# Performance work log

Measured on AMD Instinct MI355X. Metric: run time of the kernel, lower is better.

## Reference

```python
import jax, jax.numpy as jnp
import numpy as np


def setup_inputs() -> dict:
    key = jax.random.key(0)
    k1, k2 = jax.random.split(key)
    B, C, H, W_ = 16, 512, 64, 64
    x = jax.random.normal(k1, (B, C, H, W_), dtype=jnp.float32)
    W = jax.random.normal(k2, (C, C), dtype=jnp.float32) * (1.0 / np.sqrt(C))
    return {"x": x, "W": W}


def reference(x, W):
    B, C, H, Wd = x.shape
    hw = H * Wd
    x1 = x.reshape(B, C, hw)                      # [B, C, HW]
    # linearW applied to x1^T: [B, HW, C] @ W^T -> [B, HW, C]
    x1_corr = jnp.einsum('bch,dc->bhd', x1, W)    # [B, HW, C]
    s = jnp.einsum('bch,bhd->bcd', x1, x1_corr)   # [B, C, C]
    a = jax.nn.softmax(s, axis=2)
    a = jax.nn.softmax(a, axis=1)
    out = jnp.einsum('bcd,bdh->bch', a, x1) + x1  # [B, C, HW]
    return out.reshape(B, C, H, Wd)
```

## Files before the change

kernel.cpp:

```cpp
#include <hip/hip_runtime.h>


typedef __attribute__((ext_vector_type(8))) short bf16x8;
typedef __attribute__((ext_vector_type(4))) float f32x4;

#define DEVINL __device__ __forceinline__
#define CFENCE() asm volatile("" ::: "memory")

DEVINL unsigned short f2bf(float f) {
  union { float f; unsigned int u; } c; c.f = f;
  unsigned int u = c.u;
  u += 0x7fffu + ((u >> 16) & 1u);
  return (unsigned short)(u >> 16);
}

DEVINL float bf2f(unsigned short h) {
  union { unsigned int u; float f; } c; c.u = ((unsigned int)h) << 16;
  return c.f;
}

DEVINL void gld_lds16(const unsigned short* g, unsigned short* l) {
  __builtin_amdgcn_global_load_lds(
      (const __attribute__((address_space(1))) unsigned int*)g,
      (__attribute__((address_space(3))) unsigned int*)l,
      16 , 0, 0);
}

template<int N> DEVINL void vm_wait() {
  if constexpr (N == 0)       asm volatile("s_waitcnt vmcnt(0)" ::: "memory");
  else if constexpr (N == 2)  asm volatile("s_waitcnt vmcnt(2)" ::: "memory");
  else if constexpr (N == 4)  asm volatile("s_waitcnt vmcnt(4)" ::: "memory");
  else if constexpr (N == 8)  asm volatile("s_waitcnt vmcnt(8)" ::: "memory");
  else static_assert(N < 0, "unsupported vmcnt");
}

DEVINL void sym_tile_decode(int t, int& tm, int& tn) {
  if (t < 4)      { tm = 0; tn = t; }
  else if (t < 7) { tm = 1; tn = t - 3; }
  else if (t < 9) { tm = 2; tn = t - 5; }
  else            { tm = 3; tn = 3; }
}

__global__ __launch_bounds__(256)
void cvt_kernel(const float* __restrict__ in, unsigned short* __restrict__ out, int n4) {
  int i = blockIdx.x * 256 + threadIdx.x;
  const int stride = gridDim.x * 256;
  for (; i < n4; i += stride) {
    float4 v = ((const float4*)in)[i];
    unsigned int lo = (unsigned int)f2bf(v.x) | ((unsigned int)f2bf(v.y) << 16);
    unsigned int hi = (unsigned int)f2bf(v.z) | ((unsigned int)f2bf(v.w) << 16);
    uint2 o; o.x = lo; o.y = hi;
    ((uint2*)out)[i] = o;
  }
}

__global__ __launch_bounds__(256)
void fused_cvt_transpose(const float* __restrict__ x, unsigned short* __restrict__ x_bf,
                         unsigned short* __restrict__ xT) {
  __shared__ unsigned int T[2][32][68];
  const int tid = threadIdx.x;
  const int b  = blockIdx.y;
  const int hs = blockIdx.x & 31;
  const int ct = blockIdx.x >> 5;
  const int h0 = hs * 128;
  const int hq = tid & 7;
  const int c2 = tid >> 3;

  uint4 pa[2], pb[2];
  long long rowA[2];
  #pragma unroll
  for (int hh = 0; hh < 2; ++hh) {
    const int hcol = h0 + hh * 64 + hq * 8;
    rowA[hh] = (long long)(b * 512 + ct * 64 + 2 * c2) * 4096 + hcol;
    float4 a0 = *(const float4*)(x + rowA[hh]);
    float4 a1 = *(const float4*)(x + rowA[hh] + 4);
    float4 b0 = *(const float4*)(x + rowA[hh] + 4096);
    float4 b1 = *(const float4*)(x + rowA[hh] + 4100);
    unsigned short ha[8], hb[8];
    ha[0]=f2bf(a0.x); ha[1]=f2bf(a0.y); ha[2]=f2bf(a0.z); ha[3]=f2bf(a0.w);
    ha[4]=f2bf(a1.x); ha[5]=f2bf(a1.y); ha[6]=f2bf(a1.z); ha[7]=f2bf(a1.w);
    hb[0]=f2bf(b0.x); hb[1]=f2bf(b0.y); hb[2]=f2bf(b0.z); hb[3]=f2bf(b0.w);
    hb[4]=f2bf(b1.x); hb[5]=f2bf(b1.y); hb[6]=f2bf(b1.z); hb[7]=f2bf(b1.w);
    pa[hh].x = (unsigned int)ha[0] | ((unsigned int)ha[1] << 16);
    pa[hh].y = (unsigned int)ha[2] | ((unsigned int)ha[3] << 16);
    pa[hh].z = (unsigned int)ha[4] | ((unsigned int)ha[5] << 16);
    pa[hh].w = (unsigned int)ha[6] | ((unsigned int)ha[7] << 16);
    pb[hh].x = (unsigned int)hb[0] | ((unsigned int)hb[1] << 16);
    pb[hh].y = (unsigned int)hb[2] | ((unsigned int)hb[3] << 16);
    pb[hh].z = (unsigned int)hb[4] | ((unsigned int)hb[5] << 16);
    pb[hh].w = (unsigned int)hb[6] | ((unsigned int)hb[7] << 16);
    uint4 u0, u1;
    u0.x = (unsigned int)ha[0] | ((unsigned int)hb[0] << 16);
    u0.y = (unsigned int)ha[1] | ((unsigned int)hb[1] << 16);
    u0.z = (unsigned int)ha[2] | ((unsigned int)hb[2] << 16);
    u0.w = (unsigned int)ha[3] | ((unsigned int)hb[3] << 16);
    u1.x = (unsigned int)ha[4] | ((unsigned int)hb[4] << 16);
    u1.y = (unsigned int)ha[5] | ((unsigned int)hb[5] << 16);
    u1.z = (unsigned int)ha[6] | ((unsigned int)hb[6] << 16);
    u1.w = (unsigned int)ha[7] | ((unsigned int)hb[7] << 16);
    *(uint4*)&T[hh][c2][hq * 8]     = u0;
    *(uint4*)&T[hh][c2][hq * 8 + 4] = u1;
  }
  asm volatile("s_waitcnt lgkmcnt(0)" ::: "memory");
  __builtin_amdgcn_s_barrier();
  #pragma unroll
  for (int hh = 0; hh < 2; ++hh) {
    *(uint4*)(x_bf + rowA[hh])        = pa[hh];
    *(uint4*)(x_bf + rowA[hh] + 4096) = pb[hh];
  }
  const int hh2 = tid >> 7;
  const int h4  = (tid >> 3) & 15;
  const int c8  = tid & 7;
  unsigned int rv[4][4];
  #pragma unroll
  for (int i = 0; i < 4; ++i) {
    uint4 t = *(const uint4*)&T[hh2][c8 * 4 + i][h4 * 4];
    rv[i][0] = t.x; rv[i][1] = t.y; rv[i][2] = t.z; rv[i][3] = t.w;
  }
  #pragma unroll
  for (int r = 0; r < 4; ++r) {
    uint4 o;
    o.x = rv[0][r]; o.y = rv[1][r]; o.z = rv[2][r]; o.w = rv[3][r];
    *(uint4*)(xT + ((long long)(b * 4096 + h0 + hh2 * 64 + h4 * 4 + r) * 512
                    + ct * 64 + c8 * 8)) = o;
  }
}

__global__ __launch_bounds__(256)
void gemm_gsym(const unsigned short* __restrict__ X, unsigned short* __restrict__ P) {
  constexpr int HALF = 128 * 32;
  __shared__ unsigned short As[3 * HALF];
  __shared__ unsigned short Bs[3 * HALF];
  const int tid = threadIdx.x;
  const int l   = tid & 63;
  const int w   = tid >> 6;
  const int wr  = w >> 1, wc = w & 1;
  const int b   = blockIdx.y;
  const int t   = blockIdx.x >> 2;
  const int split = blockIdx.x & 3;
  int tm, tn; sym_tile_decode(t, tm, tn);

  const unsigned short* Ab = X + (long long)b * 2097152 + (long long)(tm * 128) * 4096;
  const unsigned short* Bb = X + (long long)b * 2097152 + (long long)(tn * 128) * 4096;

  f32x4 acc[4][4];
  #pragma unroll
  for (int m = 0; m < 4; ++m)
    #pragma unroll
    for (int n = 0; n < 4; ++n) acc[m][n] = (f32x4){0.f, 0.f, 0.f, 0.f};

  const int srow = tid >> 2;
  const int scol = ((tid & 3) ^ ((tid >> 3) & 3)) * 8;
  const int ch8  = (((l >> 4) ^ ((l >> 1) & 3)) * 8);

  auto stage = [&](int buf, int k0) {
    #pragma unroll
    for (int i = 0; i < 2; ++i)
      gld_lds16(Ab + (long long)(i * 64 + srow) * 4096 + k0 + scol, &As[buf * HALF + i * 2048 + tid * 8]);
    #pragma unroll
    for (int i = 0; i < 2; ++i)
      gld_lds16(Bb + (long long)(i * 64 + srow) * 4096 + k0 + scol, &Bs[buf * HALF + i * 2048 + tid * 8]);
  };
  auto compute = [&](int buf) {
    bf16x8 af[4], bfr[4];
    #pragma unroll
    for (int m = 0; m < 4; ++m)
      af[m] = *(const bf16x8*)&As[buf * HALF + (wr * 64 + m * 16 + (l & 15)) * 32 + ch8];
    #pragma unroll
    for (int n = 0; n < 4; ++n)
      bfr[n] = *(const bf16x8*)&Bs[buf * HALF + (wc * 64 + n * 16 + (l & 15)) * 32 + ch8];
    __builtin_amdgcn_s_setprio(1);
    #pragma unroll
    for (int m = 0; m < 4; ++m)
      #pragma unroll
      for (int n = 0; n < 4; ++n)
        acc[m][n] = __builtin_amdgcn_mfma_f32_16x16x32_bf16(af[m], bfr[n], acc[m][n], 0, 0, 0);
    __builtin_amdgcn_s_setprio(0);
  };

  const int k_beg = split * 1024;
  constexpr int NK = 32;
  stage(0, k_beg);
  stage(1, k_beg + 32);
  int cb = 0, sbuf = 2, ks = k_beg + 64;
  for (int k = 0; k < NK - 2; ++k) {
    stage(sbuf, ks);
    ks += 32;
    sbuf = (sbuf == 2) ? 0 : sbuf + 1;
    vm_wait<8>();
    CFENCE(); __builtin_amdgcn_s_barrier(); CFENCE();
    compute(cb);
    CFENCE(); __builtin_amdgcn_s_barrier(); CFENCE();
    cb = (cb == 2) ? 0 : cb + 1;
  }
  vm_wait<4>();
  CFENCE(); __builtin_amdgcn_s_barrier(); CFENCE();
  compute(cb);
  cb = (cb == 2) ? 0 : cb + 1;
  vm_wait<0>();
  CFENCE(); __builtin_amdgcn_s_barrier(); CFENCE();
  compute(cb);

  unsigned short* Pt = P + (((long long)b * 10 + t) * 4 + split) * 16384;
  const int cc = l & 15, r4 = (l >> 4) * 4;
  #pragma unroll
  for (int m = 0; m < 4; ++m) {
    #pragma unroll
    for (int n = 0; n < 4; ++n) {
      const int row = wr * 64 + m * 16 + r4;
      const int col = wc * 64 + n * 16 + cc;
      #pragma unroll
      for (int j = 0; j < 4; ++j)
        Pt[(row + j) * 128 + col] = f2bf(acc[m][n][j]);
    }
  }
}

__global__ __launch_bounds__(256)
void reduce_mirror(const unsigned short* __restrict__ P, unsigned short* __restrict__ G) {
  __shared__ unsigned short T[128 * 129];
  const int tid = threadIdx.x;
  const int b = blockIdx.y;
  const int t = blockIdx.x;
  int tm, tn; sym_tile_decode(t, tm, tn);
  const unsigned short* Pt = P + ((long long)(b * 10 + t) * 4) * 16384;
  unsigned short* Gb = G + (long long)b * 262144;

  #pragma unroll
  for (int e = 0; e < 16; ++e) {
    const int v = e * 256 + tid;
    ushort4 s0 = ((const ushort4*)Pt)[v];
    ushort4 s1 = ((const ushort4*)(Pt + 16384))[v];
    ushort4 s2 = ((const ushort4*)(Pt + 32768))[v];
    ushort4 s3 = ((const ushort4*)(Pt + 49152))[v];
    unsigned int h0 = f2bf(bf2f(s0.x) + bf2f(s1.x) + bf2f(s2.x) + bf2f(s3.x));
    unsigned int h1 = f2bf(bf2f(s0.y) + bf2f(s1.y) + bf2f(s2.y) + bf2f(s3.y));
    unsigned int h2 = f2bf(bf2f(s0.z) + bf2f(s1.z) + bf2f(s2.z) + bf2f(s3.z));
    unsigned int h3 = f2bf(bf2f(s0.w) + bf2f(s1.w) + bf2f(s2.w) + bf2f(s3.w));
    const int idx = v * 4;
    const int r = idx >> 7, c = idx & 127;
    unsigned int* gp = (unsigned int*)(Gb + (long long)(tm * 128 + r) * 512 + tn * 128 + c);
    gp[0] = h0 | (h1 << 16);
    gp[1] = h2 | (h3 << 16);
    unsigned short* tp = &T[r * 129 + c];
    tp[0] = (unsigned short)h0; tp[1] = (unsigned short)h1;
    tp[2] = (unsigned short)h2; tp[3] = (unsigned short)h3;
  }
  if (tm != tn) {
    __syncthreads();
    #pragma unroll
    for (int e = 0; e < 16; ++e) {
      const int idx = (e * 256 + tid) * 4;
      const int r = idx >> 7, c = idx & 127;
      unsigned int o0 = T[(c + 0) * 129 + r], o1 = T[(c + 1) * 129 + r];
      unsigned int o2 = T[(c + 2) * 129 + r], o3 = T[(c + 3) * 129 + r];
      unsigned int* gp = (unsigned int*)(Gb + (long long)(tn * 128 + r) * 512 + tm * 128 + c);
      gp[0] = o0 | (o1 << 16);
      gp[1] = o2 | (o3 << 16);
    }
  }
}

template<int FR>
__global__ __launch_bounds__(256)
void gemm_bt4(const unsigned short* __restrict__ A, const unsigned short* __restrict__ B,
              float* __restrict__ C,
              int N, int K, int sA, int sB,
              long long bsA, long long bsB, long long bsC, int Ntiles) {
  constexpr int BMN = FR * 32;
  constexpr int ISS = BMN / 64;
  constexpr int HALF = BMN * 32;
  constexpr int NLOAD = 2 * ISS;
  __shared__ unsigned short As[3 * HALF];
  __shared__ unsigned short Bs[3 * HALF];

  const int tid = threadIdx.x;
  const int l   = tid & 63;
  const int w   = tid >> 6;
  const int wr  = w >> 1, wc = w & 1;
  const int bz  = blockIdx.y;
  const int tm  = blockIdx.x / Ntiles;
  const int tn  = blockIdx.x % Ntiles;

  const unsigned short* Ab = A + bz * bsA + (long long)(tm * BMN) * sA;
  const unsigned short* Bb = B + bz * bsB + (long long)(tn * BMN) * sB;

  f32x4 acc[FR][FR];
  #pragma unroll
  for (int m = 0; m < FR; ++m)
    #pragma unroll
    for (int n = 0; n < FR; ++n) acc[m][n] = (f32x4){0.f, 0.f, 0.f, 0.f};

  const int srow = tid >> 2;
  const int scol = ((tid & 3) ^ ((tid >> 3) & 3)) * 8;
  const int ch8  = (((l >> 4) ^ ((l >> 1) & 3)) * 8);

  auto stage = [&](int buf, int k0) {
    #pragma unroll
    for (int i = 0; i < ISS; ++i)
      gld_lds16(Ab + (long long)(i * 64 + srow) * sA + k0 + scol, &As[buf * HALF + i * 2048 + tid * 8]);
    #pragma unroll
    for (int i = 0; i < ISS; ++i)
      gld_lds16(Bb + (long long)(i * 64 + srow) * sB + k0 + scol, &Bs[buf * HALF + i * 2048 + tid * 8]);
  };
  auto compute = [&](int buf) {
    bf16x8 af[FR], bfr[FR];
    #pragma unroll
    for (int m = 0; m < FR; ++m)
      af[m] = *(const bf16x8*)&As[buf * HALF + (wr * (FR * 16) + m * 16 + (l & 15)) * 32 + ch8];
    #pragma unroll
    for (int n = 0; n < FR; ++n)
      bfr[n] = *(const bf16x8*)&Bs[buf * HALF + (wc * (FR * 16) + n * 16 + (l & 15)) * 32 + ch8];
    __builtin_amdgcn_s_setprio(1);
    #pragma unroll
    for (int m = 0; m < FR; ++m)
      #pragma unroll
      for (int n = 0; n < FR; ++n)
        acc[m][n] = __builtin_amdgcn_mfma_f32_16x16x32_bf16(af[m], bfr[n], acc[m][n], 0, 0, 0);
    __builtin_amdgcn_s_setprio(0);
  };

  const int nk = K >> 5;
  stage(0, 0);
  stage(1, 32);
  int cb = 0, sbuf = 2, ks = 64;
  for (int k = 0; k < nk - 2; ++k) {
    stage(sbuf, ks);
    ks += 32;
    sbuf = (sbuf == 2) ? 0 : sbuf + 1;
    vm_wait<2 * NLOAD>();
    CFENCE(); __builtin_amdgcn_s_barrier(); CFENCE();
    compute(cb);
    CFENCE(); __builtin_amdgcn_s_barrier(); CFENCE();
    cb = (cb == 2) ? 0 : cb + 1;
  }
  vm_wait<NLOAD>();
  CFENCE(); __builtin_amdgcn_s_barrier(); CFENCE();
  compute(cb);
  cb = (cb == 2) ? 0 : cb + 1;
  vm_wait<0>();
  CFENCE(); __builtin_amdgcn_s_barrier(); CFENCE();
  compute(cb);

  const int cc = l & 15, r4 = (l >> 4) * 4;
  const int row0 = tm * BMN + wr * (FR * 16);
  const int col0 = tn * BMN + wc * (FR * 16);
  #pragma unroll
  for (int m = 0; m < FR; ++m) {
    #pragma unroll
    for (int n = 0; n < FR; ++n) {
      const int row = row0 + m * 16 + r4;
      const int col = col0 + n * 16 + cc;
      long long base = bz * bsC + (long long)row * N + col;
      #pragma unroll
      for (int j = 0; j < 4; ++j)
        C[base + (long long)j * N] = acc[m][n][j];
    }
  }
}

__global__ __launch_bounds__(256)
void row_softmax_kernel(const float* __restrict__ s, unsigned short* __restrict__ p_bf) {
  __shared__ float red[4], red2[4];
  const float* p = s + (long long)blockIdx.x * 512;
  unsigned short* q = p_bf + (long long)blockIdx.x * 512;
  const int tid = threadIdx.x;
  float v0 = p[tid], v1 = p[tid + 256];
  float m = fmaxf(v0, v1);
  #pragma unroll
  for (int i = 1; i < 64; i <<= 1) m = fmaxf(m, __shfl_xor(m, i));
  if ((tid & 63) == 0) red[tid >> 6] = m;
  __syncthreads();
  m = fmaxf(fmaxf(red[0], red[1]), fmaxf(red[2], red[3]));
  float e0 = __expf(v0 - m), e1 = __expf(v1 - m);
  float sum = e0 + e1;
  #pragma unroll
  for (int i = 1; i < 64; i <<= 1) sum += __shfl_xor(sum, i);
  if ((tid & 63) == 0) red2[tid >> 6] = sum;
  __syncthreads();
  sum = (red2[0] + red2[1]) + (red2[2] + red2[3]);
  float inv = 1.0f / sum;
  q[tid] = f2bf(e0 * inv);
  q[tid + 256] = f2bf(e1 * inv);
}

__global__ __launch_bounds__(256)
void col_softmax_kernel(const unsigned short* __restrict__ p_bf, unsigned short* __restrict__ a_bf) {
  __shared__ float cs[8][32];
  const int tid = threadIdx.x;
  const int dl = tid & 31;
  const int st = tid >> 5;
  const int d  = blockIdx.x * 32 + dl;
  const long long base = (long long)blockIdx.y * 262144 + d;
  const unsigned short* p = p_bf + base;
  float sum = 0.f;
  #pragma unroll 4
  for (int c = st * 64; c < st * 64 + 64; ++c)
    sum += __expf(bf2f(p[(long long)c * 512]));
  cs[st][dl] = sum;
  __syncthreads();
  if (st == 0) {
    float s = ((cs[0][dl] + cs[1][dl]) + (cs[2][dl] + cs[3][dl]))
            + ((cs[4][dl] + cs[5][dl]) + (cs[6][dl] + cs[7][dl]));
    cs[0][dl] = 1.0f / s;
  }
  __syncthreads();
  const float inv = cs[0][dl];
  unsigned short* q = a_bf + base;
  #pragma unroll 4
  for (int c = st * 64; c < st * 64 + 64; ++c) {
    float v = __expf(bf2f(p[(long long)c * 512])) * inv;
    if (c == d) v += 1.0f;
    q[(long long)c * 512] = f2bf(v);
  }
}

extern "C" void kernel_launch(void* const* d_in, const int* in_sizes, int n_in,
                              void* d_out, int out_size, void* d_ws, size_t ws_size,
                              hipStream_t stream) {
  (void)in_sizes; (void)n_in; (void)out_size; (void)ws_size;
  const float* x = (const float*)d_in[0];
  const float* W = (const float*)d_in[1];
  float* out = (float*)d_out;
  char* ws = (char*)d_ws;

  unsigned short* x_bf = (unsigned short*)d_out;
  unsigned short* P = (unsigned short*)((char*)d_out + 67108864);
  unsigned short* p_bf = (unsigned short*)((char*)d_out + 88080384);

  unsigned short* xT   = (unsigned short*)ws;
  unsigned short* G_bf = (unsigned short*)(ws + 67108864);
  float*          s_f  = (float*)(ws + 75497472);
  unsigned short* W_bf = (unsigned short*)(ws + 92274688);
  unsigned short* a_bf = G_bf;

  fused_cvt_transpose<<<dim3(256, 16), 256, 0, stream>>>(x, x_bf, xT);
  cvt_kernel<<<256, 256, 0, stream>>>(W, W_bf, 65536);

  gemm_gsym<<<dim3(40, 16), 256, 0, stream>>>(x_bf, P);

  reduce_mirror<<<dim3(10, 16), 256, 0, stream>>>(P, G_bf);

  gemm_bt4<2><<<dim3(64, 16), 256, 0, stream>>>(
      G_bf, W_bf, s_f,
      512, 512, 512, 512, 262144LL, 0LL, 262144LL, 8);

  row_softmax_kernel<<<8192, 256, 0, stream>>>(s_f, p_bf);
  col_softmax_kernel<<<dim3(16, 16), 256, 0, stream>>>(p_bf, a_bf);

  gemm_bt4<4><<<dim3(128, 16), 256, 0, stream>>>(
      a_bf, xT, out,
      4096, 512, 512, 512, 262144LL, 2097152LL, 2097152LL, 32);
}
```

Before: 183.9 us.

## Switch GEMM pipelines to double-buffered LDS and add nontemporal stores

The two GEMM kernels (gemm_gsym and gemm_bt4) move from a three-buffer shared-memory ring to two buffers. Each iteration now waits for the current tile, computes it, then issues the load for the tile two steps ahead into the buffer it just freed. This cuts LDS use per block, which can let more blocks run on each CU, but leaves less time to hide global-load latency. Separately, the transposed-x writes and the final large fp32 output writes now use nontemporal stores to reduce cache pollution from write-once streams.

```diff
diff --git a/kernel.cpp b/kernel.cpp
--- a/kernel.cpp
+++ b/kernel.cpp
@@ -3,6 +3,7 @@
 
 typedef __attribute__((ext_vector_type(8))) short bf16x8;
 typedef __attribute__((ext_vector_type(4))) float f32x4;
+typedef __attribute__((ext_vector_type(4))) unsigned int u32x4;
 
 #define DEVINL __device__ __forceinline__
 #define CFENCE() asm volatile("" ::: "memory")
@@ -119,18 +120,18 @@
   }
   #pragma unroll
   for (int r = 0; r < 4; ++r) {
-    uint4 o;
-    o.x = rv[0][r]; o.y = rv[1][r]; o.z = rv[2][r]; o.w = rv[3][r];
-    *(uint4*)(xT + ((long long)(b * 4096 + h0 + hh2 * 64 + h4 * 4 + r) * 512
-                    + ct * 64 + c8 * 8)) = o;
+    u32x4 o = { rv[0][r], rv[1][r], rv[2][r], rv[3][r] };
+    __builtin_nontemporal_store(o,
+        (u32x4*)(xT + ((long long)(b * 4096 + h0 + hh2 * 64 + h4 * 4 + r) * 512
+                       + ct * 64 + c8 * 8)));
   }
 }
 
 __global__ __launch_bounds__(256)
 void gemm_gsym(const unsigned short* __restrict__ X, unsigned short* __restrict__ P) {
   constexpr int HALF = 128 * 32;
-  __shared__ unsigned short As[3 * HALF];
-  __shared__ unsigned short Bs[3 * HALF];
+  __shared__ unsigned short As[2 * HALF];
+  __shared__ unsigned short Bs[2 * HALF];
   const int tid = threadIdx.x;
   const int l   = tid & 63;
   const int w   = tid >> 6;
@@ -182,24 +183,20 @@
   constexpr int NK = 32;
   stage(0, k_beg);
   stage(1, k_beg + 32);
-  int cb = 0, sbuf = 2, ks = k_beg + 64;
+  int ks = k_beg + 64;
   for (int k = 0; k < NK - 2; ++k) {
-    stage(sbuf, ks);
-    ks += 32;
-    sbuf = (sbuf == 2) ? 0 : sbuf + 1;
-    vm_wait<8>();
+    vm_wait<4>();
     CFENCE(); __builtin_amdgcn_s_barrier(); CFENCE();
-    compute(cb);
+    compute(k & 1);
     CFENCE(); __builtin_amdgcn_s_barrier(); CFENCE();
-    cb = (cb == 2) ? 0 : cb + 1;
+    stage(k & 1, ks); ks += 32;
   }
   vm_wait<4>();
   CFENCE(); __builtin_amdgcn_s_barrier(); CFENCE();
-  compute(cb);
-  cb = (cb == 2) ? 0 : cb + 1;
+  compute((NK - 2) & 1);
   vm_wait<0>();
   CFENCE(); __builtin_amdgcn_s_barrier(); CFENCE();
-  compute(cb);
+  compute((NK - 1) & 1);
 
   unsigned short* Pt = P + (((long long)b * 10 + t) * 4 + split) * 16384;
   const int cc = l & 15, r4 = (l >> 4) * 4;
@@ -261,7 +258,7 @@
   }
 }
 
-template<int FR>
+template<int FR, int NT>
 __global__ __launch_bounds__(256)
 void gemm_bt4(const unsigned short* __restrict__ A, const unsigned short* __restrict__ B,
               float* __restrict__ C,
@@ -271,8 +268,8 @@
   constexpr int ISS = BMN / 64;
   constexpr int HALF = BMN * 32;
   constexpr int NLOAD = 2 * ISS;
-  __shared__ unsigned short As[3 * HALF];
-  __shared__ unsigned short Bs[3 * HALF];
+  __shared__ unsigned short As[2 * HALF];
+  __shared__ unsigned short Bs[2 * HALF];
 
   const int tid = threadIdx.x;
   const int l   = tid & 63;
@@ -323,24 +320,20 @@
   const int nk = K >> 5;
   stage(0, 0);
   stage(1, 32);
-  int cb = 0, sbuf = 2, ks = 64;
+  int ks = 64;
   for (int k = 0; k < nk - 2; ++k) {
-    stage(sbuf, ks);
-    ks += 32;
-    sbuf = (sbuf == 2) ? 0 : sbuf + 1;
-    vm_wait<2 * NLOAD>();
+    vm_wait<NLOAD>();
     CFENCE(); __builtin_amdgcn_s_barrier(); CFENCE();
-    compute(cb);
+    compute(k & 1);
     CFENCE(); __builtin_amdgcn_s_barrier(); CFENCE();
-    cb = (cb == 2) ? 0 : cb + 1;
+    stage(k & 1, ks); ks += 32;
   }
   vm_wait<NLOAD>();
   CFENCE(); __builtin_amdgcn_s_barrier(); CFENCE();
-  compute(cb);
-  cb = (cb == 2) ? 0 : cb + 1;
+  compute(nk & 1);
   vm_wait<0>();
   CFENCE(); __builtin_amdgcn_s_barrier(); CFENCE();
-  compute(cb);
+  compute((nk - 1) & 1);
 
   const int cc = l & 15, r4 = (l >> 4) * 4;
   const int row0 = tm * BMN + wr * (FR * 16);
@@ -353,8 +346,10 @@
       const int col = col0 + n * 16 + cc;
       long long base = bz * bsC + (long long)row * N + col;
       #pragma unroll
-      for (int j = 0; j < 4; ++j)
-        C[base + (long long)j * N] = acc[m][n][j];
+      for (int j = 0; j < 4; ++j) {
+        if constexpr (NT) __builtin_nontemporal_store(acc[m][n][j], &C[base + (long long)j * N]);
+        else              C[base + (long long)j * N] = acc[m][n][j];
+      }
     }
   }
 }
@@ -441,14 +436,14 @@
 
   reduce_mirror<<<dim3(10, 16), 256, 0, stream>>>(P, G_bf);
 
-  gemm_bt4<2><<<dim3(64, 16), 256, 0, stream>>>(
+  gemm_bt4<2, 0><<<dim3(64, 16), 256, 0, stream>>>(
       G_bf, W_bf, s_f,
       512, 512, 512, 512, 262144LL, 0LL, 262144LL, 8);
 
   row_softmax_kernel<<<8192, 256, 0, stream>>>(s_f, p_bf);
   col_softmax_kernel<<<dim3(16, 16), 256, 0, stream>>>(p_bf, a_bf);
 
-  gemm_bt4<4><<<dim3(128, 16), 256, 0, stream>>>(
+  gemm_bt4<4, 1><<<dim3(128, 16), 256, 0, stream>>>(
       a_bf, xT, out,
       4096, 512, 512, 512, 262144LL, 2097152LL, 2097152LL, 32);
 }
```

Result: no change. 184.4 us (+0.3%).
